# Kernel optimization log

Hardware: AMD Instinct MI355X
Metric: run time of the kernel (lower is better)

Reference implementation:

```python
import jax, jax.numpy as jnp
import numpy as np

B, T, NTR, NTE = 16, 256, 1024, 256
K0, L0 = 1, 1   # torus T1 ensemble
K1, L1 = 16, 2  # euclidean R2 ensemble


def angle2vector(a):
    return jnp.stack([jnp.sin(a), jnp.cos(a)], axis=-1)


def get_grid(latent_dim, num_basis):
    n = int(round(num_basis ** (1.0 / latent_dim)))
    pts = np.linspace(-np.pi, np.pi, n, endpoint=False)
    grid = np.stack(np.meshgrid(*([pts] * latent_dim), indexing='ij'), axis=-1)
    return jnp.asarray(grid.reshape(1, num_basis, latent_dim), jnp.float32)


def gauss_response(z, rf, coeff, mean, log_var, manifold):
    # z: (B,T,L)  rf: (N,L)  coeff: (1,K)  mean: (1,K,L)  log_var: (1,K,L)
    if manifold == 'torus':
        z = angle2vector(z)        # (B,T,L,2)
        rf = angle2vector(rf)      # (N,L,2)
        mean = angle2vector(mean)  # (1,K,L,2)
        sum_axes = (4, 5)
    else:
        sum_axes = (4,)
    mean = mean - rf[:, None]                  # (N,K,L[,2])
    dist = z[:, :, None, None] - mean[None, None]   # (B,T,N,K,L[,2])
    dist = dist / jnp.exp(log_var)[None, None]
    dist = jnp.sum(dist ** 2, axis=sum_axes)        # (B,T,N,K)
    resp = jnp.sum(jnp.exp(-dist) * coeff[None, None], axis=3)  # (B,T,N)
    return jnp.exp(resp)  # nonlinearity='exp'


def setup_inputs() -> dict:
    key = jax.random.key(0)
    ks = jax.random.split(key, 12)
    two_pi = 2.0 * np.pi
    z0 = jax.random.uniform(ks[0], (B, T, L0), jnp.float32) * two_pi - np.pi
    z1 = jax.random.normal(ks[1], (B, T, L1), jnp.float32)
    # FeatureBasis params (shared=True -> leading dim 1)
    coeff0 = jax.random.normal(ks[2], (1, K0), jnp.float32) * 0.01
    coeff0 = coeff0.at[:, 0].add(1.0)
    mean0 = get_grid(L0, K0)
    log_var0 = jnp.log(jnp.ones((1, K0, L0), jnp.float32) * 10.0)
    coeff1 = jax.random.normal(ks[3], (1, K1), jnp.float32) * 0.01
    coeff1 = coeff1.at[:, 0].add(1.0)
    mean1 = get_grid(L1, K1)
    log_var1 = jnp.log(jnp.ones((1, K1, L1), jnp.float32) * 10.0)
    # receptive fields: torus -> uniform angles, euclidean -> randn
    rf_tr0 = jax.random.uniform(ks[4], (NTR, L0), jnp.float32) * two_pi - np.pi
    rf_te0 = jax.random.uniform(ks[5], (NTE, L0), jnp.float32) * two_pi - np.pi
    rf_tr1 = jax.random.normal(ks[6], (NTR, L1), jnp.float32)
    rf_te1 = jax.random.normal(ks[7], (NTE, L1), jnp.float32)
    ew_tr = jax.random.normal(ks[8], (NTR, 2), jnp.float32)
    ew_te = jax.random.normal(ks[9], (NTE, 2), jnp.float32)
    lfs_tr = jnp.zeros((NTR,), jnp.float32)
    lfs_te = jnp.zeros((NTE,), jnp.float32)
    return dict(z0=z0, z1=z1, coeff0=coeff0, mean0=mean0, log_var0=log_var0,
                coeff1=coeff1, mean1=mean1, log_var1=log_var1,
                rf_tr0=rf_tr0, rf_tr1=rf_tr1, rf_te0=rf_te0, rf_te1=rf_te1,
                ew_tr=ew_tr, ew_te=ew_te, lfs_tr=lfs_tr, lfs_te=lfs_te)


def reference(z0, z1, coeff0, mean0, log_var0, coeff1, mean1, log_var1,
              rf_tr0, rf_tr1, rf_te0, rf_te1, ew_tr, ew_te, lfs_tr, lfs_te):
    sg = jax.lax.stop_gradient
    r_tr = jnp.stack([
        gauss_response(z0, rf_tr0, coeff0, mean0, log_var0, 'torus'),
        gauss_response(z1, rf_tr1, coeff1, mean1, log_var1, 'euclidean'),
    ], axis=3)  # (B,T,NTR,2)
    # shared=True -> test responses use train basis with detached z and basis params
    r_te = jnp.stack([
        gauss_response(sg(z0), rf_te0, sg(coeff0), sg(mean0), sg(log_var0), 'torus'),
        gauss_response(sg(z1), rf_te1, sg(coeff1), sg(mean1), sg(log_var1), 'euclidean'),
    ], axis=3)  # (B,T,NTE,2)
    w_tr = jax.nn.softmax(ew_tr, axis=1)[None, None]
    w_te = jax.nn.softmax(ew_te, axis=1)[None, None]
    out_tr = jnp.sum(w_tr * r_tr, axis=3) * jnp.exp(lfs_tr)[None, None]
    out_te = jnp.sum(w_te * r_te, axis=3) * jnp.exp(lfs_te)[None, None]
    return out_tr.transpose(0, 2, 1), out_te.transpose(0, 2, 1)  # (B,N,T)
```

## Files before the change

kernel.cpp:

```cpp
#include <hip/hip_runtime.h>
#include <math.h>

#define B_ 16
#define T_ 256
#define NTR_ 1024
#define NTE_ 256
#define K1_ 16

__global__ __launch_bounds__(256) void decoder_kernel(
    const float* __restrict__ z0,
    const float* __restrict__ z1,
    const float* __restrict__ coeff0,
    const float* __restrict__ mean0,
    const float* __restrict__ log_var0,
    const float* __restrict__ coeff1,
    const float* __restrict__ mean1,
    const float* __restrict__ log_var1,
    const float* __restrict__ rf_tr0,
    const float* __restrict__ rf_tr1,
    const float* __restrict__ rf_te0,
    const float* __restrict__ rf_te1,
    const float* __restrict__ ew_tr,
    const float* __restrict__ ew_te,
    const float* __restrict__ lfs_tr,
    const float* __restrict__ lfs_te,
    float* __restrict__ out)
{
    int bid = blockIdx.x;
    int t = threadIdx.x;

    const float *rf0, *rf1, *ew, *lfs;
    float* obase;
    int N, lbid;
    if (bid < B_ * NTR_) {
        rf0 = rf_tr0; rf1 = rf_tr1; ew = ew_tr; lfs = lfs_tr;
        obase = out;
        N = NTR_; lbid = bid;
    } else {
        rf0 = rf_te0; rf1 = rf_te1; ew = ew_te; lfs = lfs_te;
        obase = out + (size_t)B_ * NTR_ * T_;
        N = NTE_; lbid = bid - B_ * NTR_;
    }
    int n = lbid % N;
    int b = lbid / N;

    __shared__ float s_mux[K1_], s_muy[K1_], s_isx[K1_], s_isy[K1_], s_ck[K1_];
    __shared__ float s_sc[8];
    if (t < K1_) {
        float rfx = rf1[n * 2 + 0];
        float rfy = rf1[n * 2 + 1];
        s_mux[t] = mean1[t * 2 + 0] - rfx;
        s_muy[t] = mean1[t * 2 + 1] - rfy;
        s_isx[t] = __expf(-log_var1[t * 2 + 0]);
        s_isy[t] = __expf(-log_var1[t * 2 + 1]);
        s_ck[t]  = coeff1[t];
    }
    if (t == 0) {
        float srf, crf;
        __sincosf(rf0[n], &srf, &crf);
        float sm, cm;
        __sincosf(mean0[0], &sm, &cm);
        s_sc[0] = sm - srf;
        s_sc[1] = cm - crf;
        s_sc[2] = __expf(-log_var0[0]);
        s_sc[3] = coeff0[0];
        float e0 = ew[n * 2 + 0], e1 = ew[n * 2 + 1];
        float mx = fmaxf(e0, e1);
        float x0 = __expf(e0 - mx), x1 = __expf(e1 - mx);
        float inv = 1.0f / (x0 + x1);
        s_sc[4] = x0 * inv;
        s_sc[5] = x1 * inv;
        s_sc[6] = __expf(lfs[n]);
    }
    __syncthreads();

    int zt = b * T_ + t;
    float zs, zc;
    __sincosf(z0[zt], &zs, &zc);
    float ds = (zs - s_sc[0]) * s_sc[2];
    float dc = (zc - s_sc[1]) * s_sc[2];
    float dist0 = ds * ds + dc * dc;
    float r0 = __expf(__expf(-dist0) * s_sc[3]);

    float2 zv = ((const float2*)z1)[zt];
    float resp = 0.0f;
#pragma unroll
    for (int k = 0; k < K1_; ++k) {
        float dx = (zv.x - s_mux[k]) * s_isx[k];
        float dy = (zv.y - s_muy[k]) * s_isy[k];
        float d = dx * dx + dy * dy;
        resp = __fmaf_rn(__expf(-d), s_ck[k], resp);
    }
    float r1 = __expf(resp);

    obase[(size_t)lbid * T_ + t] = (s_sc[4] * r0 + s_sc[5] * r1) * s_sc[6];
}

extern "C" void kernel_launch(void* const* d_in, const int* in_sizes, int n_in,
                              void* d_out, int out_size, void* d_ws, size_t ws_size,
                              hipStream_t stream) {
    const float* z0       = (const float*)d_in[0];
    const float* z1       = (const float*)d_in[1];
    const float* coeff0   = (const float*)d_in[2];
    const float* mean0    = (const float*)d_in[3];
    const float* log_var0 = (const float*)d_in[4];
    const float* coeff1   = (const float*)d_in[5];
    const float* mean1    = (const float*)d_in[6];
    const float* log_var1 = (const float*)d_in[7];
    const float* rf_tr0   = (const float*)d_in[8];
    const float* rf_tr1   = (const float*)d_in[9];
    const float* rf_te0   = (const float*)d_in[10];
    const float* rf_te1   = (const float*)d_in[11];
    const float* ew_tr    = (const float*)d_in[12];
    const float* ew_te    = (const float*)d_in[13];
    const float* lfs_tr   = (const float*)d_in[14];
    const float* lfs_te   = (const float*)d_in[15];
    float* out = (float*)d_out;

    int grid = B_ * (NTR_ + NTE_);
    decoder_kernel<<<grid, T_, 0, stream>>>(
        z0, z1, coeff0, mean0, log_var0, coeff1, mean1, log_var1,
        rf_tr0, rf_tr1, rf_te0, rf_te1, ew_tr, ew_te, lfs_tr, lfs_te, out);
}
```

Measured before the change: 120.4 us.

## Expand Gaussian quadratics into exp2 FMAs and loop batch inside each block

Each block now handles all 16 batch rows for one neuron, so the per-neuron setup (shared-memory basis constants, softmax, sincos of the receptive field) is computed once rather than per batch. The Gaussian distance is expanded into a polynomial in z with precomputed coefficients and fed to a native exp2, using the unit norm of the sin/cos vector on the torus side. The intent is to cut the per-element ALU and transcendental work and the redundant block setup. In exchange the grid shrinks 16-fold to 1280 blocks, each with more registers and serial work, and the expanded quadratic may lose some precision through cancellation.

```diff
diff --git a/kernel.cpp b/kernel.cpp
--- a/kernel.cpp
+++ b/kernel.cpp
@@ -6,6 +6,7 @@
 #define NTR_ 1024
 #define NTE_ 256
 #define K1_ 16
+#define LOG2E_ 1.44269504088896340736f
 
 __global__ __launch_bounds__(256) void decoder_kernel(
     const float* __restrict__ z0,
@@ -26,74 +27,99 @@
     const float* __restrict__ lfs_te,
     float* __restrict__ out)
 {
-    int bid = blockIdx.x;
-    int t = threadIdx.x;
+    const int bid = blockIdx.x;
+    const int t = threadIdx.x;
 
     const float *rf0, *rf1, *ew, *lfs;
     float* obase;
-    int N, lbid;
-    if (bid < B_ * NTR_) {
+    int N, n;
+    if (bid < NTR_) {
         rf0 = rf_tr0; rf1 = rf_tr1; ew = ew_tr; lfs = lfs_tr;
         obase = out;
-        N = NTR_; lbid = bid;
+        N = NTR_; n = bid;
     } else {
         rf0 = rf_te0; rf1 = rf_te1; ew = ew_te; lfs = lfs_te;
         obase = out + (size_t)B_ * NTR_ * T_;
-        N = NTE_; lbid = bid - B_ * NTR_;
+        N = NTE_; n = bid - NTR_;
     }
-    int n = lbid % N;
-    int b = lbid / N;
 
-    __shared__ float s_mux[K1_], s_muy[K1_], s_isx[K1_], s_isy[K1_], s_ck[K1_];
+    __shared__ float s_ax[K1_], s_bx[K1_], s_ay[K1_], s_by[K1_], s_c[K1_], s_ck[K1_];
     __shared__ float s_sc[8];
     if (t < K1_) {
         float rfx = rf1[n * 2 + 0];
         float rfy = rf1[n * 2 + 1];
-        s_mux[t] = mean1[t * 2 + 0] - rfx;
-        s_muy[t] = mean1[t * 2 + 1] - rfy;
-        s_isx[t] = __expf(-log_var1[t * 2 + 0]);
-        s_isy[t] = __expf(-log_var1[t * 2 + 1]);
-        s_ck[t]  = coeff1[t];
+        float mux = mean1[t * 2 + 0] - rfx;
+        float muy = mean1[t * 2 + 1] - rfy;
+        float ivx = __expf(-log_var1[t * 2 + 0]);
+        float ivy = __expf(-log_var1[t * 2 + 1]);
+        float gx = ivx * ivx * LOG2E_;
+        float gy = ivy * ivy * LOG2E_;
+        s_ax[t] = -gx;
+        s_bx[t] = 2.0f * gx * mux;
+        s_ay[t] = -gy;
+        s_by[t] = 2.0f * gy * muy;
+        s_c[t]  = -gx * mux * mux - gy * muy * muy;
+        s_ck[t] = coeff1[t] * LOG2E_;
     }
     if (t == 0) {
         float srf, crf;
         __sincosf(rf0[n], &srf, &crf);
         float sm, cm;
         __sincosf(mean0[0], &sm, &cm);
-        s_sc[0] = sm - srf;
-        s_sc[1] = cm - crf;
-        s_sc[2] = __expf(-log_var0[0]);
-        s_sc[3] = coeff0[0];
+        float s0 = sm - srf;
+        float s1 = cm - crf;
+        float iv = __expf(-log_var0[0]);
+        float q = iv * iv * LOG2E_;
+        s_sc[0] = s0;
+        s_sc[1] = s1;
+        s_sc[2] = -q * (1.0f + s0 * s0 + s1 * s1);
+        s_sc[3] = 2.0f * q;
+        s_sc[4] = coeff0[0] * LOG2E_;
         float e0 = ew[n * 2 + 0], e1 = ew[n * 2 + 1];
         float mx = fmaxf(e0, e1);
         float x0 = __expf(e0 - mx), x1 = __expf(e1 - mx);
-        float inv = 1.0f / (x0 + x1);
-        s_sc[4] = x0 * inv;
-        s_sc[5] = x1 * inv;
-        s_sc[6] = __expf(lfs[n]);
+        float elfs = __expf(lfs[n]) / (x0 + x1);
+        s_sc[5] = x0 * elfs;
+        s_sc[6] = x1 * elfs;
     }
     __syncthreads();
 
-    int zt = b * T_ + t;
-    float zs, zc;
-    __sincosf(z0[zt], &zs, &zc);
-    float ds = (zs - s_sc[0]) * s_sc[2];
-    float dc = (zc - s_sc[1]) * s_sc[2];
-    float dist0 = ds * ds + dc * dc;
-    float r0 = __expf(__expf(-dist0) * s_sc[3]);
+    float zx[B_], zy[B_], resp[B_];
+    const float2* z1v = (const float2*)z1;
+#pragma unroll
+    for (int b = 0; b < B_; ++b) {
+        float2 zv = z1v[b * T_ + t];
+        zx[b] = zv.x;
+        zy[b] = zv.y;
+        resp[b] = 0.0f;
+    }
 
-    float2 zv = ((const float2*)z1)[zt];
-    float resp = 0.0f;
 #pragma unroll
     for (int k = 0; k < K1_; ++k) {
-        float dx = (zv.x - s_mux[k]) * s_isx[k];
-        float dy = (zv.y - s_muy[k]) * s_isy[k];
-        float d = dx * dx + dy * dy;
-        resp = __fmaf_rn(__expf(-d), s_ck[k], resp);
+        float ax = s_ax[k], bx = s_bx[k];
+        float ay = s_ay[k], by = s_by[k];
+        float c = s_c[k], ck = s_ck[k];
+#pragma unroll
+        for (int b = 0; b < B_; ++b) {
+            float e = __fmaf_rn(zx[b], __fmaf_rn(zx[b], ax, bx),
+                     __fmaf_rn(zy[b], __fmaf_rn(zy[b], ay, by), c));
+            resp[b] = __fmaf_rn(__builtin_amdgcn_exp2f(e), ck, resp[b]);
+        }
     }
-    float r1 = __expf(resp);
 
-    obase[(size_t)lbid * T_ + t] = (s_sc[4] * r0 + s_sc[5] * r1) * s_sc[6];
+    const float s0 = s_sc[0], s1 = s_sc[1], Cn = s_sc[2], Dn = s_sc[3];
+    const float E = s_sc[4], w0p = s_sc[5], w1p = s_sc[6];
+
+#pragma unroll
+    for (int b = 0; b < B_; ++b) {
+        float zs, zc;
+        __sincosf(z0[b * T_ + t], &zs, &zc);
+        float dot = __fmaf_rn(zc, s1, zs * s0);
+        float r0 = __builtin_amdgcn_exp2f(
+            __builtin_amdgcn_exp2f(__fmaf_rn(dot, Dn, Cn)) * E);
+        float r1 = __builtin_amdgcn_exp2f(resp[b]);
+        obase[(size_t)(b * N + n) * T_ + t] = __fmaf_rn(w0p, r0, w1p * r1);
+    }
 }
 
 extern "C" void kernel_launch(void* const* d_in, const int* in_sizes, int n_in,
@@ -117,7 +143,7 @@
     const float* lfs_te   = (const float*)d_in[15];
     float* out = (float*)d_out;
 
-    int grid = B_ * (NTR_ + NTE_);
+    int grid = NTR_ + NTE_;
     decoder_kernel<<<grid, T_, 0, stream>>>(
         z0, z1, coeff0, mean0, log_var0, coeff1, mean1, log_var1,
         rf_tr0, rf_tr1, rf_te0, rf_te1, ew_tr, ew_te, lfs_tr, lfs_te, out);
```

Result: faster. 112.8 us (-6.2%).
